# Performance work log

Measured on AMD Instinct MI355X. Metric: run time of the kernel, lower is better.

Reference implementation:

```python
import jax, jax.numpy as jnp
import numpy as np

N_NODES = 50000
N_EDGES = 25000
NNZ = 800000
IN_DIM = 256
OUT_DIM = 256


def setup_inputs() -> dict:
    key = jax.random.key(0)
    k1, k2, k3, k4, k5 = jax.random.split(key, 5)
    X = jax.random.normal(k1, (N_NODES, IN_DIM), dtype=jnp.float32)
    node_idx = jax.random.randint(k2, (NNZ,), 0, N_NODES, dtype=jnp.int64)
    edge_idx = jax.random.randint(k3, (NNZ,), 0, N_EDGES, dtype=jnp.int64)
    # Xavier-uniform-ish weight, zero bias (matches reset_parameters)
    limit = float(np.sqrt(6.0 / (IN_DIM + OUT_DIM)))
    W = jax.random.uniform(k4, (IN_DIM, OUT_DIM), dtype=jnp.float32, minval=-limit, maxval=limit)
    b = jnp.zeros((OUT_DIM,), dtype=jnp.float32)
    return {"X": X, "node_idx": node_idx, "edge_idx": edge_idx, "W": W, "b": b}


def reference(X, node_idx, edge_idx, W, b):
    # Y = X @ W + b  -- dense GEMM
    Y = X @ W + b  # [N, out_dim]

    ones = jnp.ones(node_idx.shape[0], dtype=Y.dtype)
    # D_v = rowsum(H)^-0.5 (inf -> 0); D_e = colsum(H)^-1 (inf -> 0)
    deg_v = jax.ops.segment_sum(ones, node_idx, num_segments=N_NODES)
    deg_e = jax.ops.segment_sum(ones, edge_idx, num_segments=N_EDGES)
    d_v = jnp.where(deg_v > 0, deg_v ** -0.5, 0.0)  # [N]
    d_e = jnp.where(deg_e > 0, 1.0 / deg_e, 0.0)    # [E]

    # step1 = H^T @ (D_v X): gather scaled node rows, scatter-add into edges
    Z = d_v[:, None] * Y                                   # [N, out_dim]
    step1 = jax.ops.segment_sum(Z[node_idx], edge_idx, num_segments=N_EDGES)  # [E, out_dim]
    # step2 = D_e @ step1
    step2 = d_e[:, None] * step1                           # [E, out_dim]
    # step3 = H @ step2: gather edge rows, scatter-add into nodes
    step3 = jax.ops.segment_sum(step2[edge_idx], node_idx, num_segments=N_NODES)  # [N, out_dim]
    # final = D_v @ step3
    return d_v[:, None] * step3
```

## Files before the change

### kernel.cpp

```cpp
#include <hip/hip_runtime.h>

#define N_NODES 50000
#define N_EDGES 25000
#define NNZ     800000
#define DIM     256

#define CAP_E 88
#define CAP_V 56

#define NBE 98
#define NBV 196
#define CE_COARSE 8800
#define CV_COARSE 4500
#define NNZ_PB 2048
#define P1_BLOCKS 391

#define B_A1   0
#define B_CE   0
#define B_CV   3449600
#define B_CSRE 12800000
#define B_CSRV 17200000
#define B_WT   22800000
#define B_CURV 22931072
#define B_CURE 23131072
#define B_S1B  23231072
#define B_CCUR 23331072

typedef __attribute__((ext_vector_type(8))) short s8v;
typedef __attribute__((ext_vector_type(4))) float f4v;

__device__ __forceinline__ unsigned short f2bf(float f) {
    unsigned u = __float_as_uint(f);
    u = (u + 0x7FFFu + ((u >> 16) & 1u)) >> 16;
    return (unsigned short)u;
}
__device__ __forceinline__ float bf2f(unsigned short h) {
    return __uint_as_float(((unsigned)h) << 16);
}

__global__ __launch_bounds__(256) void k_prep(
        const float* __restrict__ X, const float* __restrict__ W,
        const int* __restrict__ node_idx, const int* __restrict__ edge_idx,
        unsigned short* __restrict__ Xb, unsigned short* __restrict__ WTb,
        unsigned* __restrict__ ccurE, unsigned* __restrict__ ccurV,
        unsigned* __restrict__ coarseE, unsigned* __restrict__ coarseV) {
    if (blockIdx.x < 6250) {
        size_t i = ((size_t)blockIdx.x * 256 + threadIdx.x) * 8;
        float4 p0 = *(const float4*)(X + i);
        float4 p1 = *(const float4*)(X + i + 4);
        unsigned short o[8] = {f2bf(p0.x), f2bf(p0.y), f2bf(p0.z), f2bf(p0.w),
                               f2bf(p1.x), f2bf(p1.y), f2bf(p1.z), f2bf(p1.w)};
        *(s8v*)(Xb + i) = *(const s8v*)o;
        return;
    }
    if (blockIdx.x < 6282) {
        int t = (blockIdx.x - 6250) * 256 + threadIdx.x;
        int n = t >> 5;
        int k0 = (t & 31) * 8;
        unsigned short o[8];
#pragma unroll
        for (int j = 0; j < 8; ++j) o[j] = f2bf(W[(size_t)(k0 + j) * DIM + n]);
        *(s8v*)(WTb + (size_t)n * DIM + k0) = *(const s8v*)o;
        return;
    }

    __shared__ unsigned histE[NBE], histV[NBV], baseE[NBE], baseV[NBV];
    const int tid = threadIdx.x;
    const int pb  = blockIdx.x - 6282;
    const int base = pb * NNZ_PB;

    if (tid < NBE) histE[tid] = 0;
    if (tid < NBV) histV[tid] = 0;
    __syncthreads();

    int idx0 = base + tid * 4;
    int idx1 = base + 1024 + tid * 4;
    bool ok0 = idx0 < NNZ, ok1 = idx1 < NNZ;
    int4 v0 = ok0 ? *(const int4*)(node_idx + idx0) : (int4){0,0,0,0};
    int4 e0 = ok0 ? *(const int4*)(edge_idx + idx0) : (int4){0,0,0,0};
    int4 v1 = ok1 ? *(const int4*)(node_idx + idx1) : (int4){0,0,0,0};
    int4 e1 = ok1 ? *(const int4*)(edge_idx + idx1) : (int4){0,0,0,0};
    int vv[8] = {v0.x, v0.y, v0.z, v0.w, v1.x, v1.y, v1.z, v1.w};
    int ee[8] = {e0.x, e0.y, e0.z, e0.w, e1.x, e1.y, e1.z, e1.w};

    unsigned short locE[8], locV[8];
#pragma unroll
    for (int j = 0; j < 8; ++j) {
        bool ok = (j < 4) ? ok0 : ok1;
        if (ok) {
            locE[j] = (unsigned short)atomicAdd(&histE[ee[j] >> 8], 1u);
            locV[j] = (unsigned short)atomicAdd(&histV[vv[j] >> 8], 1u);
        }
    }
    __syncthreads();
    if (tid < NBE) baseE[tid] = atomicAdd(&ccurE[tid], histE[tid]);
    if (tid < NBV) baseV[tid] = atomicAdd(&ccurV[tid], histV[tid]);
    __syncthreads();

#pragma unroll
    for (int j = 0; j < 8; ++j) {
        bool ok = (j < 4) ? ok0 : ok1;
        if (ok) {
            unsigned e = (unsigned)ee[j], v = (unsigned)vv[j];
            unsigned pe = baseE[e >> 8] + locE[j];
            if (pe < CE_COARSE)
                coarseE[(size_t)(e >> 8) * CE_COARSE + pe] = ((e & 255u) << 16) | v;
            unsigned pv = baseV[v >> 8] + locV[j];
            if (pv < CV_COARSE)
                coarseV[(size_t)(v >> 8) * CV_COARSE + pv] = ((v & 255u) << 16) | e;
        }
    }
}

__global__ __launch_bounds__(256) void k_fine(
        const unsigned* __restrict__ coarseE, const unsigned* __restrict__ coarseV,
        const unsigned* __restrict__ ccurE, const unsigned* __restrict__ ccurV,
        unsigned short* __restrict__ csrE, unsigned short* __restrict__ csrV,
        unsigned* __restrict__ cur_e, unsigned* __restrict__ cur_v) {
    __shared__ unsigned cnt[256];
    __shared__ unsigned short slots[256 * CAP_E];
    const int tid = threadIdx.x;
    cnt[tid] = 0;
    __syncthreads();

    if (blockIdx.x < NBE) {
        int b = blockIdx.x;
        unsigned n = ccurE[b]; n = n < CE_COARSE ? n : CE_COARSE;
        const unsigned* src = coarseE + (size_t)b * CE_COARSE;
        for (unsigned i = tid; i < n; i += 256) {
            unsigned p = src[i];
            unsigned f = p >> 16, v = p & 0xFFFFu;
            unsigned pos = atomicAdd(&cnt[f], 1u);
            if (pos < CAP_E) slots[f * CAP_E + pos] = (unsigned short)v;
        }
        __syncthreads();
        int e = b * 256 + tid;
        if (e < N_EDGES) cur_e[e] = cnt[tid];
        int rows = N_EDGES - b * 256; rows = rows < 256 ? rows : 256;
        unsigned words = (unsigned)rows * (CAP_E / 2);
        unsigned* dst = (unsigned*)(csrE + (size_t)b * 256 * CAP_E);
        const unsigned* s = (const unsigned*)slots;
        for (unsigned i = tid; i < words; i += 256) dst[i] = s[i];
    } else {
        int b = blockIdx.x - NBE;
        unsigned n = ccurV[b]; n = n < CV_COARSE ? n : CV_COARSE;
        const unsigned* src = coarseV + (size_t)b * CV_COARSE;
        for (unsigned i = tid; i < n; i += 256) {
            unsigned p = src[i];
            unsigned f = p >> 16, e = p & 0xFFFFu;
            unsigned pos = atomicAdd(&cnt[f], 1u);
            if (pos < CAP_V) slots[f * CAP_V + pos] = (unsigned short)e;
        }
        __syncthreads();
        int v = b * 256 + tid;
        if (v < N_NODES) cur_v[v] = cnt[tid];
        int rows = N_NODES - b * 256; rows = rows < 256 ? rows : 256;
        unsigned words = (unsigned)rows * (CAP_V / 2);
        unsigned* dst = (unsigned*)(csrV + (size_t)b * 256 * CAP_V);
        const unsigned* s = (const unsigned*)slots;
        for (unsigned i = tid; i < words; i += 256) dst[i] = s[i];
    }
}

__global__ __launch_bounds__(256) void k_gather_edges(
        const unsigned short* __restrict__ Xb,
        const unsigned short* __restrict__ csrE,
        const unsigned* __restrict__ cur_e, const unsigned* __restrict__ cur_v,
        unsigned short* __restrict__ A1, float* __restrict__ s1b) {
    int w = (blockIdx.x * 256 + threadIdx.x) >> 6;
    int lane = threadIdx.x & 63;
    if (w >= N_EDGES) return;
    unsigned cnt = cur_e[w];
    cnt = cnt < CAP_E ? cnt : CAP_E;
    const unsigned short* lst = csrE + (size_t)w * CAP_E;
    float ax = 0.f, ay = 0.f, az = 0.f, aw = 0.f, ss = 0.f;
    unsigned j = 0;
    for (; j + 2 <= cnt; j += 2) {
        int v0 = lst[j], v1 = lst[j + 1];
        float s0 = __frsqrt_rn((float)cur_v[v0]);
        float s1 = __frsqrt_rn((float)cur_v[v1]);
        ushort4 x0 = *(const ushort4*)(Xb + (size_t)v0 * DIM + lane * 4);
        ushort4 x1 = *(const ushort4*)(Xb + (size_t)v1 * DIM + lane * 4);
        ax = fmaf(s0, bf2f(x0.x), ax); ay = fmaf(s0, bf2f(x0.y), ay);
        az = fmaf(s0, bf2f(x0.z), az); aw = fmaf(s0, bf2f(x0.w), aw);
        ax = fmaf(s1, bf2f(x1.x), ax); ay = fmaf(s1, bf2f(x1.y), ay);
        az = fmaf(s1, bf2f(x1.z), az); aw = fmaf(s1, bf2f(x1.w), aw);
        ss += s0 + s1;
    }
    if (j < cnt) {
        int v = lst[j];
        float s = __frsqrt_rn((float)cur_v[v]);
        ushort4 x = *(const ushort4*)(Xb + (size_t)v * DIM + lane * 4);
        ax = fmaf(s, bf2f(x.x), ax); ay = fmaf(s, bf2f(x.y), ay);
        az = fmaf(s, bf2f(x.z), az); aw = fmaf(s, bf2f(x.w), aw);
        ss += s;
    }
    ushort4 o = {f2bf(ax), f2bf(ay), f2bf(az), f2bf(aw)};
    *(ushort4*)(A1 + (size_t)w * DIM + lane * 4) = o;
    if (lane == 0) s1b[w] = ss;
}

__global__ __launch_bounds__(256) void k_gemm_mfma(
        const unsigned short* __restrict__ A,
        const unsigned short* __restrict__ WT,
        const float* __restrict__ bias,
        const unsigned* __restrict__ cur_e,
        const float* __restrict__ s1b,
        unsigned short* __restrict__ S2) {
    const int tid  = threadIdx.x;
    const int wv   = tid >> 6;
    const int lane = tid & 63;
    const int quad = lane >> 4;
    const int l16  = lane & 15;
    const int r0   = blockIdx.x * 64;
    const int nb   = wv * 64;

    f4v acc[4][4];
#pragma unroll
    for (int mt = 0; mt < 4; ++mt)
#pragma unroll
        for (int nt = 0; nt < 4; ++nt) acc[mt][nt] = (f4v){0.f, 0.f, 0.f, 0.f};

    for (int k0 = 0; k0 < DIM; k0 += 32) {
        s8v a[4], b[4];
#pragma unroll
        for (int nt = 0; nt < 4; ++nt) {
            int n = nb + nt * 16 + l16;
            b[nt] = *(const s8v*)(WT + (size_t)n * DIM + k0 + quad * 8);
        }
#pragma unroll
        for (int mt = 0; mt < 4; ++mt) {
            int m = r0 + mt * 16 + l16;
            m = (m < N_EDGES) ? m : (N_EDGES - 1);
            a[mt] = *(const s8v*)(A + (size_t)m * DIM + k0 + quad * 8);
        }
#pragma unroll
        for (int mt = 0; mt < 4; ++mt)
#pragma unroll
            for (int nt = 0; nt < 4; ++nt)
                acc[mt][nt] = __builtin_amdgcn_mfma_f32_16x16x32_bf16(
                    a[mt], b[nt], acc[mt][nt], 0, 0, 0);
    }

    __syncthreads();

    float bv[4];
#pragma unroll
    for (int nt = 0; nt < 4; ++nt) bv[nt] = bias[nb + nt * 16 + l16];

#pragma unroll
    for (int mt = 0; mt < 4; ++mt) {
#pragma unroll
        for (int reg = 0; reg < 4; ++reg) {
            int row = r0 + mt * 16 + quad * 4 + reg;
            if (row < N_EDGES) {
                unsigned ce = cur_e[row];
                float sc = ce ? 1.0f / (float)ce : 0.0f;
                float sb = s1b[row];
#pragma unroll
                for (int nt = 0; nt < 4; ++nt) {
                    float v = sc * (acc[mt][nt][reg] + sb * bv[nt]);
                    S2[(size_t)row * DIM + nb + nt * 16 + l16] = f2bf(v);
                }
            }
        }
    }
}

__global__ __launch_bounds__(256) void k_gather_nodes(
        const unsigned short* __restrict__ S2,
        const unsigned short* __restrict__ csrV,
        const unsigned* __restrict__ cur_v,
        float* __restrict__ out) {
    int w = (blockIdx.x * 256 + threadIdx.x) >> 6;
    int lane = threadIdx.x & 63;
    if (w >= N_NODES) return;
    unsigned cnt = cur_v[w];
    float s = cnt ? __frsqrt_rn((float)cnt) : 0.0f;
    cnt = cnt < CAP_V ? cnt : CAP_V;
    const unsigned short* lst = csrV + (size_t)w * CAP_V;
    float ax = 0.f, ay = 0.f, az = 0.f, aw = 0.f;
    unsigned j = 0;
    for (; j + 2 <= cnt; j += 2) {
        int e0 = lst[j], e1 = lst[j + 1];
        ushort4 a = *(const ushort4*)(S2 + (size_t)e0 * DIM + lane * 4);
        ushort4 b = *(const ushort4*)(S2 + (size_t)e1 * DIM + lane * 4);
        ax += bf2f(a.x) + bf2f(b.x); ay += bf2f(a.y) + bf2f(b.y);
        az += bf2f(a.z) + bf2f(b.z); aw += bf2f(a.w) + bf2f(b.w);
    }
    if (j < cnt) {
        int e = lst[j];
        ushort4 a = *(const ushort4*)(S2 + (size_t)e * DIM + lane * 4);
        ax += bf2f(a.x); ay += bf2f(a.y); az += bf2f(a.z); aw += bf2f(a.w);
    }
    float4 o = {s * ax, s * ay, s * az, s * aw};
    *(float4*)(out + (size_t)w * DIM + lane * 4) = o;
}

extern "C" void kernel_launch(void* const* d_in, const int* in_sizes, int n_in,
                              void* d_out, int out_size, void* d_ws, size_t ws_size,
                              hipStream_t stream) {
    (void)in_sizes; (void)n_in; (void)out_size; (void)ws_size;
    const float* X        = (const float*)d_in[0];
    const int*   node_idx = (const int*)d_in[1];
    const int*   edge_idx = (const int*)d_in[2];
    const float* W        = (const float*)d_in[3];
    const float* bias     = (const float*)d_in[4];
    float* out = (float*)d_out;
    char*  ws  = (char*)d_ws;

    unsigned short* A1      = (unsigned short*)(ws + B_A1);
    unsigned*       coarseE = (unsigned*)(ws + B_CE);
    unsigned*       coarseV = (unsigned*)(ws + B_CV);
    unsigned short* csrE    = (unsigned short*)(ws + B_CSRE);
    unsigned short* csrV    = (unsigned short*)(ws + B_CSRV);
    unsigned short* WTb     = (unsigned short*)(ws + B_WT);
    unsigned*       cur_v   = (unsigned*)(ws + B_CURV);
    unsigned*       cur_e   = (unsigned*)(ws + B_CURE);
    float*          s1b     = (float*)(ws + B_S1B);
    unsigned*       ccurE   = (unsigned*)(ws + B_CCUR);
    unsigned*       ccurV   = ccurE + NBE;

    unsigned short* Xb = (unsigned short*)d_out;

    hipMemsetAsync(ccurE, 0, (NBE + NBV) * sizeof(unsigned), stream);

    k_prep<<<6282 + P1_BLOCKS, 256, 0, stream>>>(X, W, node_idx, edge_idx,
                                                 Xb, WTb, ccurE, ccurV, coarseE, coarseV);
    k_fine<<<NBE + NBV, 256, 0, stream>>>(coarseE, coarseV, ccurE, ccurV,
                                          csrE, csrV, cur_e, cur_v);
    k_gather_edges<<<(N_EDGES * 64 + 255) / 256, 256, 0, stream>>>(
        Xb, csrE, cur_e, cur_v, A1, s1b);
    k_gemm_mfma<<<(N_EDGES + 63) / 64, 256, 0, stream>>>(A1, WTb, bias, cur_e, s1b, A1);
    k_gather_nodes<<<(N_NODES * 64 + 255) / 256, 256, 0, stream>>>(A1, csrV, cur_v, out);
}
```

Baseline: 283.6 us.

## Slice gather kernels by feature column and precompute node degree scales

Both gather kernels now split the 256-wide feature dimension into 8 slices of 32 columns, one slice per block. Each row is handled by 16 lanes loading ushort2, replacing a full wave loading ushort4, and consecutive blocks cover different slices of the same rows. This is meant to shrink the working set of concurrently gathered columns and improve cache locality. Node scales d_v are computed once in k_fine and stored to a new buffer, so the per-neighbour rsqrt and cur_v lookup go away. The trade-off is 8x more blocks, narrower memory accesses, and the index lists and counts being reread once per slice.

```diff
diff --git a/kernel.cpp b/kernel.cpp
--- a/kernel.cpp
+++ b/kernel.cpp
@@ -25,6 +25,7 @@
 #define B_CURE 23131072
 #define B_S1B  23231072
 #define B_CCUR 23331072
+#define B_DV   23332248
 
 typedef __attribute__((ext_vector_type(8))) short s8v;
 typedef __attribute__((ext_vector_type(4))) float f4v;
@@ -116,7 +117,8 @@
         const unsigned* __restrict__ coarseE, const unsigned* __restrict__ coarseV,
         const unsigned* __restrict__ ccurE, const unsigned* __restrict__ ccurV,
         unsigned short* __restrict__ csrE, unsigned short* __restrict__ csrV,
-        unsigned* __restrict__ cur_e, unsigned* __restrict__ cur_v) {
+        unsigned* __restrict__ cur_e, unsigned* __restrict__ cur_v,
+        float* __restrict__ dv) {
     __shared__ unsigned cnt[256];
     __shared__ unsigned short slots[256 * CAP_E];
     const int tid = threadIdx.x;
@@ -153,7 +155,11 @@
         }
         __syncthreads();
         int v = b * 256 + tid;
-        if (v < N_NODES) cur_v[v] = cnt[tid];
+        if (v < N_NODES) {
+            unsigned c = cnt[tid];
+            cur_v[v] = c;
+            dv[v] = c ? __frsqrt_rn((float)c) : 0.0f;
+        }
         int rows = N_NODES - b * 256; rows = rows < 256 ? rows : 256;
         unsigned words = (unsigned)rows * (CAP_V / 2);
         unsigned* dst = (unsigned*)(csrV + (size_t)b * 256 * CAP_V);
@@ -165,39 +171,39 @@
 __global__ __launch_bounds__(256) void k_gather_edges(
         const unsigned short* __restrict__ Xb,
         const unsigned short* __restrict__ csrE,
-        const unsigned* __restrict__ cur_e, const unsigned* __restrict__ cur_v,
+        const unsigned* __restrict__ cur_e,
+        const float* __restrict__ dv,
         unsigned short* __restrict__ A1, float* __restrict__ s1b) {
-    int w = (blockIdx.x * 256 + threadIdx.x) >> 6;
-    int lane = threadIdx.x & 63;
-    if (w >= N_EDGES) return;
-    unsigned cnt = cur_e[w];
-    cnt = cnt < CAP_E ? cnt : CAP_E;
-    const unsigned short* lst = csrE + (size_t)w * CAP_E;
-    float ax = 0.f, ay = 0.f, az = 0.f, aw = 0.f, ss = 0.f;
+    const int slice = blockIdx.x & 7;
+    const int chunk = blockIdx.x >> 3;
+    const int g = threadIdx.x >> 4;
+    const int l = threadIdx.x & 15;
+    const int e = chunk * 16 + g;
+    if (e >= N_EDGES) return;
+    unsigned cnt = cur_e[e]; cnt = cnt < CAP_E ? cnt : CAP_E;
+    const unsigned short* lst = csrE + (size_t)e * CAP_E;
+    const unsigned dof = slice * 32 + l * 2;
+    float a0 = 0.f, a1 = 0.f, ss = 0.f;
     unsigned j = 0;
     for (; j + 2 <= cnt; j += 2) {
         int v0 = lst[j], v1 = lst[j + 1];
-        float s0 = __frsqrt_rn((float)cur_v[v0]);
-        float s1 = __frsqrt_rn((float)cur_v[v1]);
-        ushort4 x0 = *(const ushort4*)(Xb + (size_t)v0 * DIM + lane * 4);
-        ushort4 x1 = *(const ushort4*)(Xb + (size_t)v1 * DIM + lane * 4);
-        ax = fmaf(s0, bf2f(x0.x), ax); ay = fmaf(s0, bf2f(x0.y), ay);
-        az = fmaf(s0, bf2f(x0.z), az); aw = fmaf(s0, bf2f(x0.w), aw);
-        ax = fmaf(s1, bf2f(x1.x), ax); ay = fmaf(s1, bf2f(x1.y), ay);
-        az = fmaf(s1, bf2f(x1.z), az); aw = fmaf(s1, bf2f(x1.w), aw);
+        float s0 = dv[v0], s1 = dv[v1];
+        ushort2 x0 = *(const ushort2*)(Xb + (size_t)v0 * DIM + dof);
+        ushort2 x1 = *(const ushort2*)(Xb + (size_t)v1 * DIM + dof);
+        a0 = fmaf(s0, bf2f(x0.x), a0); a1 = fmaf(s0, bf2f(x0.y), a1);
+        a0 = fmaf(s1, bf2f(x1.x), a0); a1 = fmaf(s1, bf2f(x1.y), a1);
         ss += s0 + s1;
     }
     if (j < cnt) {
         int v = lst[j];
-        float s = __frsqrt_rn((float)cur_v[v]);
-        ushort4 x = *(const ushort4*)(Xb + (size_t)v * DIM + lane * 4);
-        ax = fmaf(s, bf2f(x.x), ax); ay = fmaf(s, bf2f(x.y), ay);
-        az = fmaf(s, bf2f(x.z), az); aw = fmaf(s, bf2f(x.w), aw);
+        float s = dv[v];
+        ushort2 x = *(const ushort2*)(Xb + (size_t)v * DIM + dof);
+        a0 = fmaf(s, bf2f(x.x), a0); a1 = fmaf(s, bf2f(x.y), a1);
         ss += s;
     }
-    ushort4 o = {f2bf(ax), f2bf(ay), f2bf(az), f2bf(aw)};
-    *(ushort4*)(A1 + (size_t)w * DIM + lane * 4) = o;
-    if (lane == 0) s1b[w] = ss;
+    ushort2 o = {f2bf(a0), f2bf(a1)};
+    *(ushort2*)(A1 + (size_t)e * DIM + dof) = o;
+    if (slice == 0 && l == 0) s1b[e] = ss;
 }
 
 __global__ __launch_bounds__(256) void k_gemm_mfma(
@@ -271,30 +277,34 @@
         const unsigned short* __restrict__ S2,
         const unsigned short* __restrict__ csrV,
         const unsigned* __restrict__ cur_v,
+        const float* __restrict__ dv,
         float* __restrict__ out) {
-    int w = (blockIdx.x * 256 + threadIdx.x) >> 6;
-    int lane = threadIdx.x & 63;
-    if (w >= N_NODES) return;
-    unsigned cnt = cur_v[w];
-    float s = cnt ? __frsqrt_rn((float)cnt) : 0.0f;
-    cnt = cnt < CAP_V ? cnt : CAP_V;
-    const unsigned short* lst = csrV + (size_t)w * CAP_V;
-    float ax = 0.f, ay = 0.f, az = 0.f, aw = 0.f;
+    const int slice = blockIdx.x & 7;
+    const int chunk = blockIdx.x >> 3;
+    const int g = threadIdx.x >> 4;
+    const int l = threadIdx.x & 15;
+    const int v = chunk * 16 + g;
+    if (v >= N_NODES) return;
+    unsigned cnt = cur_v[v]; cnt = cnt < CAP_V ? cnt : CAP_V;
+    const unsigned short* lst = csrV + (size_t)v * CAP_V;
+    const unsigned dof = slice * 32 + l * 2;
+    float a0 = 0.f, a1 = 0.f;
     unsigned j = 0;
     for (; j + 2 <= cnt; j += 2) {
         int e0 = lst[j], e1 = lst[j + 1];
-        ushort4 a = *(const ushort4*)(S2 + (size_t)e0 * DIM + lane * 4);
-        ushort4 b = *(const ushort4*)(S2 + (size_t)e1 * DIM + lane * 4);
-        ax += bf2f(a.x) + bf2f(b.x); ay += bf2f(a.y) + bf2f(b.y);
-        az += bf2f(a.z) + bf2f(b.z); aw += bf2f(a.w) + bf2f(b.w);
+        ushort2 x0 = *(const ushort2*)(S2 + (size_t)e0 * DIM + dof);
+        ushort2 x1 = *(const ushort2*)(S2 + (size_t)e1 * DIM + dof);
+        a0 += bf2f(x0.x) + bf2f(x1.x);
+        a1 += bf2f(x0.y) + bf2f(x1.y);
     }
     if (j < cnt) {
         int e = lst[j];
-        ushort4 a = *(const ushort4*)(S2 + (size_t)e * DIM + lane * 4);
-        ax += bf2f(a.x); ay += bf2f(a.y); az += bf2f(a.z); aw += bf2f(a.w);
-    }
-    float4 o = {s * ax, s * ay, s * az, s * aw};
-    *(float4*)(out + (size_t)w * DIM + lane * 4) = o;
+        ushort2 x = *(const ushort2*)(S2 + (size_t)e * DIM + dof);
+        a0 += bf2f(x.x); a1 += bf2f(x.y);
+    }
+    float s = dv[v];
+    float2 o = {s * a0, s * a1};
+    *(float2*)(out + (size_t)v * DIM + dof) = o;
 }
 
 extern "C" void kernel_launch(void* const* d_in, const int* in_sizes, int n_in,
@@ -320,6 +330,7 @@
     float*          s1b     = (float*)(ws + B_S1B);
     unsigned*       ccurE   = (unsigned*)(ws + B_CCUR);
     unsigned*       ccurV   = ccurE + NBE;
+    float*          dv      = (float*)(ws + B_DV);
 
     unsigned short* Xb = (unsigned short*)d_out;
 
@@ -328,9 +339,10 @@
     k_prep<<<6282 + P1_BLOCKS, 256, 0, stream>>>(X, W, node_idx, edge_idx,
                                                  Xb, WTb, ccurE, ccurV, coarseE, coarseV);
     k_fine<<<NBE + NBV, 256, 0, stream>>>(coarseE, coarseV, ccurE, ccurV,
-                                          csrE, csrV, cur_e, cur_v);
-    k_gather_edges<<<(N_EDGES * 64 + 255) / 256, 256, 0, stream>>>(
-        Xb, csrE, cur_e, cur_v, A1, s1b);
+                                          csrE, csrV, cur_e, cur_v, dv);
+    k_gather_edges<<<((N_EDGES + 15) / 16) * 8, 256, 0, stream>>>(
+        Xb, csrE, cur_e, dv, A1, s1b);
     k_gemm_mfma<<<(N_EDGES + 63) / 64, 256, 0, stream>>>(A1, WTb, bias, cur_e, s1b, A1);
-    k_gather_nodes<<<(N_NODES * 64 + 255) / 256, 256, 0, stream>>>(A1, csrV, cur_v, out);
-}
+    k_gather_nodes<<<((N_NODES + 15) / 16) * 8, 256, 0, stream>>>(
+        A1, csrV, cur_v, dv, out);
+}
```

Measured after the change: 372.0 us. +31.2%, slower.
